# Performance work log

Measured on AMD Instinct MI355X. Metric: run time of the kernel, lower is better.

## Reference

```python
import jax, jax.numpy as jnp
import numpy as np

HEADS = 4
NEG_SLOPE = 0.2  # GATv2Conv default negative_slope and module's LeakyReLU
LN_EPS = 1e-5


def setup_inputs() -> dict:
    key = jax.random.key(0)
    ks = jax.random.split(key, 12)
    N, D, E = 50000, 128, 400000
    H, C = HEADS, D
    s = 0.05
    x = jax.random.normal(ks[0], (N, D), dtype=jnp.float32)
    edge_index = jax.random.randint(ks[1], (2, E), 0, N, dtype=jnp.int64)
    return {
        "x": x,
        "edge_index": edge_index,
        "W_l": jax.random.normal(ks[2], (D, H * C), dtype=jnp.float32) * s,
        "b_l": jnp.zeros((H * C,), jnp.float32),
        "W_r": jax.random.normal(ks[3], (D, H * C), dtype=jnp.float32) * s,
        "b_r": jnp.zeros((H * C,), jnp.float32),
        "att": jax.random.normal(ks[4], (H, C), dtype=jnp.float32) * s,
        "gat_bias": jnp.zeros((C,), jnp.float32),
        "ln_g": jnp.ones((D,), jnp.float32),
        "ln_b": jnp.zeros((D,), jnp.float32),
        "W1": jax.random.normal(ks[5], (D, 2 * D), dtype=jnp.float32) * s,
        "b1": jnp.zeros((2 * D,), jnp.float32),
        "W2": jax.random.normal(ks[6], (2 * D, D), dtype=jnp.float32) * s,
        "b2": jnp.zeros((D,), jnp.float32),
    }


def _gatv2(x, src, dst, W_l, b_l, W_r, b_r, att, gat_bias, N):
    D = x.shape[1]
    H, C = HEADS, D
    xl = (x @ W_l + b_l).reshape(N, H, C)  # source-side projection
    xr = (x @ W_r + b_r).reshape(N, H, C)  # target-side projection
    # per-edge GATv2 score: leaky_relu(x_j + x_i) . att
    e = jax.nn.leaky_relu(xl[src] + xr[dst], NEG_SLOPE)  # [E, H, C]
    alpha = jnp.einsum('ehc,hc->eh', e, att)             # [E, H]
    # segment softmax over destination nodes
    amax = jax.ops.segment_max(alpha, dst, num_segments=N)  # [N, H]
    ex = jnp.exp(alpha - amax[dst])
    denom = jax.ops.segment_sum(ex, dst, num_segments=N)
    w = ex / (denom[dst] + 1e-16)                        # [E, H]
    msg = xl[src] * w[:, :, None]                        # [E, H, C]
    out = jax.ops.segment_sum(msg, dst, num_segments=N)  # [N, H, C]
    return out.mean(axis=1) + gat_bias                   # concat=False -> head mean + bias


def reference(x, edge_index, W_l, b_l, W_r, b_r, att, gat_bias, ln_g, ln_b, W1, b1, W2, b2):
    N = x.shape[0]
    # GATv2Conv default add_self_loops=True
    loops = jnp.arange(N, dtype=edge_index.dtype)
    src = jnp.concatenate([edge_index[0], loops])
    dst = jnp.concatenate([edge_index[1], loops])
    h = x + _gatv2(x, src, dst, W_l, b_l, W_r, b_r, att, gat_bias, N)
    # LayerNorm
    mu = h.mean(-1, keepdims=True)
    var = ((h - mu) ** 2).mean(-1, keepdims=True)
    hn = (h - mu) * jax.lax.rsqrt(var + LN_EPS) * ln_g + ln_b
    # FFN with residual
    ffn = jax.nn.leaky_relu(hn @ W1 + b1, NEG_SLOPE) @ W2 + b2
    return hn + ffn
```

## Files before the change

kernel.cpp:

```cpp
#include <hip/hip_runtime.h>
#include <hip/hip_bf16.h>
#include <stdint.h>

typedef __hip_bfloat16 bf16;
typedef __attribute__((ext_vector_type(8))) short short8;
typedef __attribute__((ext_vector_type(4))) float f32x4;

#define NEG 0.2f
#define LN_EPS 1e-5f

__device__ __host__ __forceinline__ int stdch(int q) {
    return (q & ~63) | (16 * (q & 3)) | ((q & 63) >> 2);
}

__device__ __forceinline__ float bits2f(unsigned b) {
    return __uint_as_float(b << 16);
}
__device__ __forceinline__ float hi2f(unsigned b) {
    return __uint_as_float(b & 0xffff0000u);
}
__device__ __forceinline__ unsigned short f2b_bits(float f) {
    unsigned u = __float_as_uint(f);
    unsigned r = u + 0x7fffu + ((u >> 16) & 1u);
    return (unsigned short)(r >> 16);
}
__device__ __forceinline__ float lrelu(float v) {
    return fmaxf(v, 0.f) + NEG * fminf(v, 0.f);
}
__device__ __forceinline__ void unpack8(uint4 u, float* v) {
    v[0] = bits2f(u.x); v[1] = hi2f(u.x);
    v[2] = bits2f(u.y); v[3] = hi2f(u.y);
    v[4] = bits2f(u.z); v[5] = hi2f(u.z);
    v[6] = bits2f(u.w); v[7] = hi2f(u.w);
}

union S8 { uint4 u; short8 s; unsigned short us[8]; };
__device__ __forceinline__ short8 ld8b(const char* p) {
    S8 c; c.u = *(const uint4*)p; return c.s;
}
__device__ __forceinline__ short8 ld8f(const float* p) {
    float4 a = ((const float4*)p)[0], b = ((const float4*)p)[1];
    S8 c;
    c.us[0] = f2b_bits(a.x); c.us[1] = f2b_bits(a.y);
    c.us[2] = f2b_bits(a.z); c.us[3] = f2b_bits(a.w);
    c.us[4] = f2b_bits(b.x); c.us[5] = f2b_bits(b.y);
    c.us[6] = f2b_bits(b.z); c.us[7] = f2b_bits(b.w);
    return c.s;
}

template <int CTRL>
__device__ __forceinline__ float ror_add16(float x) {
    int xi = __float_as_int(x);
    int r = __builtin_amdgcn_update_dpp(xi, xi, CTRL, 0xf, 0xf, false);
    return x + __int_as_float(r);
}

__global__ void detect_kernel(const unsigned* __restrict__ xw, const int* __restrict__ ei,
                              int* __restrict__ flags, int E) {
    int lane = threadIdx.x;
    int sane = 0;
    for (int k = 0; k < 4; ++k) {
        unsigned short lo = (unsigned short)(xw[k * 64 + lane] & 0xFFFFu);
        int ex = (lo >> 7) & 0xFF;
        if (lo == 0 || (ex > 100 && ex < 155)) sane++;
    }
#pragma unroll
    for (int off = 32; off > 0; off >>= 1) sane += __shfl_xor(sane, off);
    int nchk = E < 64 ? E : 64;
    int bad = (lane < nchk) ? (ei[2 * lane + 1] != 0) : 0;
    unsigned long long bb = __ballot(bad);
    if (lane == 0) {
        flags[0] = (sane > 200) ? 1 : 0;
        flags[1] = (bb == 0ULL) ? 1 : 0;
    }
}

struct PrepArgs {
    const void* Wl; const void* Wr; const void* W1; const void* W2;
    const void* ssrc[8];
    const int* ei;
    unsigned short* Wlt; unsigned short* Wrt; unsigned short* W1t; unsigned short* W2x;
    float* smalls;
    int* deg;
    int N; int E;
};
__device__ __forceinline__ float cvt_one(const void* p, int idx, int isb) {
    return isb ? bits2f(((const unsigned short*)p)[idx]) : ((const float*)p)[idx];
}
__global__ __launch_bounds__(256) void prep_kernel(PrepArgs a, const int* __restrict__ flags) {
    int isb = flags[0];
    int i = blockIdx.x * 256 + threadIdx.x;
    int seg = blockIdx.y;
    if (seg == 0) {
        if (i < 512 * 128) {
            int j = i & 7, lane = (i >> 3) & 63, k4 = (i >> 9) & 3, nb = i >> 11;
            int col = nb * 16 + (lane & 15);
            int k = k4 * 32 + (lane >> 4) * 8 + j;
            a.Wlt[i] = isb ? ((const unsigned short*)a.Wl)[k * 512 + col]
                           : f2b_bits(((const float*)a.Wl)[k * 512 + col]);
        }
    } else if (seg == 1) {
        if (i < 512 * 128) {
            int j = i & 7, lane = (i >> 3) & 63, k4 = (i >> 9) & 3, nb = i >> 11;
            int col = nb * 16 + (lane & 15);
            int k = k4 * 32 + (lane >> 4) * 8 + j;
            a.Wrt[i] = isb ? ((const unsigned short*)a.Wr)[k * 512 + col]
                           : f2b_bits(((const float*)a.Wr)[k * 512 + col]);
        }
    } else if (seg == 2) {
        if (i < 256 * 128) {
            int j = i & 7, lane = (i >> 3) & 63;
            int r2 = i >> 9;
            int k4 = r2 & 3, nb = r2 >> 2;
            int col = nb * 16 + (lane & 15);
            int q = k4 * 32 + (lane >> 4) * 8 + j;
            int k = stdch(q);
            a.W1t[i] = isb ? ((const unsigned short*)a.W1)[k * 256 + col]
                           : f2b_bits(((const float*)a.W1)[k * 256 + col]);
        }
    } else if (seg == 3) {
        if (i < 128 * 384) {
            int j = i & 7, lane = (i >> 3) & 63;
            int r2 = i >> 9;
            int k4 = r2 % 12, nb = r2 / 12;
            int col = nb * 16 + (lane & 15);
            int p = k4 * 32 + (lane >> 4) * 8 + j;
            if (p < 256) {
                int k = stdch(p);
                a.W2x[i] = isb ? ((const unsigned short*)a.W2)[k * 128 + col]
                               : f2b_bits(((const float*)a.W2)[k * 128 + col]);
            } else {
                int q = p - 256;
                a.W2x[i] = (stdch(q) == col) ? (unsigned short)0x3F80 : (unsigned short)0;
            }
        }
    } else if (seg == 4) {
        if (i < a.E) {
            int d = flags[1] ? a.ei[2 * (size_t)a.E + 2 * (size_t)i] : a.ei[(size_t)a.E + i];
            if ((unsigned)d >= (unsigned)a.N) d = 0;
            atomicAdd(&a.deg[d], 1);
        }
    } else {
        if (i < 512) a.smalls[i] = cvt_one(a.ssrc[0], i, isb);
        else if (i < 1024) a.smalls[i] = cvt_one(a.ssrc[1], i - 512, isb);
        else if (i < 1536) {
            int j = i - 1024, h = j >> 7, q = j & 127;
            a.smalls[i] = cvt_one(a.ssrc[2], h * 128 + stdch(q), isb);
        } else if (i < 1664) a.smalls[i] = cvt_one(a.ssrc[3], stdch(i - 1536), isb);
        else if (i < 1792)   a.smalls[i] = cvt_one(a.ssrc[4], stdch(i - 1664), isb);
        else if (i < 1920)   a.smalls[i] = cvt_one(a.ssrc[5], stdch(i - 1792), isb);
        else if (i < 2176)   a.smalls[i] = cvt_one(a.ssrc[6], i - 1920, isb);
        else if (i < 2304)   a.smalls[i] = cvt_one(a.ssrc[7], i - 2176, isb);
    }
}


__global__ __launch_bounds__(256) void proj_scatter_kernel(
    const void* __restrict__ xv, const unsigned short* __restrict__ Wlt,
    const unsigned short* __restrict__ Wrt, const float* __restrict__ smalls,
    unsigned short* __restrict__ xl, unsigned short* __restrict__ xr,
    const int* __restrict__ ei, int* __restrict__ cursor, int* __restrict__ srcs,
    int N, int E, int ET, int gproj, const int* __restrict__ flags) {
    if ((int)blockIdx.x >= gproj) {
        int e = ((int)blockIdx.x - gproj) * 256 + (int)threadIdx.x;
        if (e >= ET) return;
        int s, d;
        if (e < E) {
            if (flags[1]) { s = ei[2 * (size_t)e]; d = ei[2 * (size_t)E + 2 * (size_t)e]; }
            else          { s = ei[e];             d = ei[(size_t)E + e]; }
        } else { s = e - E; d = s; }
        if ((unsigned)s >= (unsigned)N) s = 0;
        if ((unsigned)d >= (unsigned)N) d = 0;
        int pos = atomicAdd(&cursor[d], 1);
        srcs[pos] = s;
        return;
    }
    __shared__ __align__(16) unsigned short alds[64 * 136];
    int isb = flags[0];
    int tt = (int)threadIdx.x;
    int wid = threadIdx.x >> 6, lane = threadIdx.x & 63;
    int quad = lane >> 4, l16 = lane & 15;
    int m0 = blockIdx.x * 64;

#pragma unroll
    for (int s = 0; s < 4; ++s) {
        int row = s * 16 + (tt >> 4);
        int gr = m0 + row; gr = (gr < N) ? gr : N - 1;
        S8 c8;
        if (isb) c8.u = *(const uint4*)((const char*)xv + (size_t)gr * 256 + (tt & 15) * 16);
        else     c8.s = ld8f((const float*)xv + (size_t)gr * 128 + (tt & 15) * 8);
        *(uint4*)(alds + row * 136 + (tt & 15) * 8) = c8.u;
    }
    __syncthreads();
    short8 A[4][4];
#pragma unroll
    for (int rf = 0; rf < 4; ++rf)
#pragma unroll
        for (int k4 = 0; k4 < 4; ++k4)
            A[rf][k4] = ld8b((const char*)(alds + (rf * 16 + l16) * 136 + k4 * 32 + quad * 8));

    for (int iter = 0; iter < 4; ++iter) {
        const unsigned short* Wt = (iter < 2) ? Wlt : Wrt;
        const float* bias = smalls + ((iter < 2) ? 0 : 512);
        unsigned short* out = (iter < 2) ? xl : xr;
        int n0 = (iter & 1) * 256 + wid * 64;
        int nb0 = n0 >> 4;

        f32x4 acc[4][4];
#pragma unroll
        for (int rf = 0; rf < 4; ++rf)
#pragma unroll
            for (int c = 0; c < 4; ++c) acc[rf][c] = (f32x4){0.f, 0.f, 0.f, 0.f};

#pragma unroll
        for (int k4 = 0; k4 < 4; ++k4) {
            short8 b[4];
#pragma unroll
            for (int c = 0; c < 4; ++c)
                b[c] = ld8b((const char*)(Wt + (((size_t)(nb0 + c) * 4 + k4) * 64 + lane) * 8));
#pragma unroll
            for (int rf = 0; rf < 4; ++rf)
#pragma unroll
                for (int c = 0; c < 4; ++c)
                    acc[rf][c] = __builtin_amdgcn_mfma_f32_16x16x32_bf16(A[rf][k4], b[c], acc[rf][c], 0, 0, 0);
        }
        float bv[4];
#pragma unroll
        for (int c = 0; c < 4; ++c) bv[c] = bias[n0 + c * 16 + l16];
#pragma unroll
        for (int rf = 0; rf < 4; ++rf) {
#pragma unroll
            for (int j = 0; j < 4; ++j) {
                int row = m0 + rf * 16 + quad * 4 + j;
                if (row < N) {
                    uint2 pk;
                    pk.x = (unsigned)f2b_bits(acc[rf][0][j] + bv[0]) |
                           ((unsigned)f2b_bits(acc[rf][1][j] + bv[1]) << 16);
                    pk.y = (unsigned)f2b_bits(acc[rf][2][j] + bv[2]) |
                           ((unsigned)f2b_bits(acc[rf][3][j] + bv[3]) << 16);
                    *(uint2*)(out + (size_t)row * 512 + n0 + 4 * l16) = pk;
                }
            }
        }
    }
}

__global__ __launch_bounds__(256) void scanA_kernel(const int* __restrict__ deg,
                                                    int* __restrict__ part, int N) {
    int t = threadIdx.x, lane = t & 63, wid = t >> 6;
    int i = blockIdx.x * 256 + t;
    int v = (i < N) ? deg[i] + 1 : 0;
#pragma unroll
    for (int off = 32; off > 0; off >>= 1) v += __shfl_xor(v, off);
    __shared__ int ws4[4];
    if (lane == 0) ws4[wid] = v;
    __syncthreads();
    if (t == 0) part[blockIdx.x] = ws4[0] + ws4[1] + ws4[2] + ws4[3];
}

__global__ __launch_bounds__(256) void scanC_kernel(const int* __restrict__ deg,
                                                    const int* __restrict__ part,
                                                    int* __restrict__ rowptr,
                                                    int* __restrict__ cursor, int N) {
    int t = threadIdx.x, lane = t & 63, wid = t >> 6;
    int b = blockIdx.x;
    __shared__ int ws[4];
    int acc = 0;
    for (int c0 = 0; c0 < b; c0 += 256) {
        int idx = c0 + t;
        int v = (idx < b) ? part[idx] : 0;
#pragma unroll
        for (int off = 32; off > 0; off >>= 1) v += __shfl_xor(v, off);
        if (lane == 0) ws[wid] = v;
        __syncthreads();
        acc += ws[0] + ws[1] + ws[2] + ws[3];
        __syncthreads();
    }
    int i = b * 256 + t;
    int v = (i < N) ? deg[i] + 1 : 0;
    int x = v;
#pragma unroll
    for (int off = 1; off < 64; off <<= 1) {
        int u = __shfl_up(x, off);
        if (lane >= off) x += u;
    }
    if (lane == 63) ws[wid] = x;
    __syncthreads();
    int base = acc;
    for (int w = 0; w < wid; ++w) base += ws[w];
    int excl = base + x - v;
    if (i < N) { rowptr[i] = excl; cursor[i] = excl; }
    if (b == (int)gridDim.x - 1 && t == 0)
        rowptr[N] = acc + ws[0] + ws[1] + ws[2] + ws[3];
}

__global__ __launch_bounds__(256, 2) void agg_kernel(
    const bf16* __restrict__ xl, bf16* __restrict__ xr,
    const void* __restrict__ xv, const int* __restrict__ rowptr,
    const int* __restrict__ srcs, const float* __restrict__ smalls,
    int N, const int* __restrict__ flags) {
    int n = blockIdx.x * 4 + (threadIdx.x >> 6);
    if (n >= N) return;
    int lane = threadIdx.x & 63;
    int h = lane >> 4, cg = lane & 15;
    const float* att = smalls + 1024;
    const float* gat_bias = smalls + 1536;
    const float* ln_g = smalls + 1664;
    const float* ln_b = smalls + 1792;

    float att_f[8];
    {
        const float4* ap = (const float4*)(att + (size_t)h * 128 + cg * 8);
        float4 a0 = ap[0], a1 = ap[1];
        att_f[0] = a0.x; att_f[1] = a0.y; att_f[2] = a0.z; att_f[3] = a0.w;
        att_f[4] = a1.x; att_f[5] = a1.y; att_f[6] = a1.z; att_f[7] = a1.w;
    }
    float xr_f[8];
    uint4 xw = ((const uint4*)(xr + (size_t)n * 512))[lane];
    unpack8(xw, xr_f);

    float o[8];
#pragma unroll
    for (int j = 0; j < 8; ++j) o[j] = 0.f;
    float lsum = 0.f;

    int beg = rowptr[n], end = rowptr[n + 1];
    int last = end - 1;
    const uint4* xlu = (const uint4*)xl;
    int sA = srcs[beg];
    int sB = srcs[min(beg + 1, last)];
    uint4 lw = xlu[(size_t)sA * 64 + lane];
    for (int i = beg; i < end; ++i) {
        uint4 cur = lw;
        int snext = sB;
        sB = srcs[min(i + 2, last)];
        lw = xlu[(size_t)snext * 64 + lane];
        float v[8];
        unpack8(cur, v);
        float dotA = 0.f, dotB = 0.f;
#pragma unroll
        for (int j = 0; j < 8; ++j) {
            float z = v[j] + xr_f[j];
            dotA = fmaf(z, att_f[j], dotA);
            dotB = fmaf(fabsf(z), att_f[j], dotB);
        }
        float p = fmaf(0.4f, dotB, 0.6f * dotA);
        p = ror_add16<0x128>(p);
        p = ror_add16<0x124>(p);
        p = ror_add16<0x122>(p);
        p = ror_add16<0x121>(p);
        float w = __expf(fminf(p, 60.f));
        lsum += w;
#pragma unroll
        for (int j = 0; j < 8; ++j) o[j] = fmaf(w, v[j], o[j]);
        asm volatile("" : "+v"(o[0]), "+v"(o[1]), "+v"(o[2]), "+v"(o[3]),
                          "+v"(o[4]), "+v"(o[5]), "+v"(o[6]), "+v"(o[7]),
                          "+v"(lsum),
                          "+v"(att_f[0]), "+v"(att_f[1]), "+v"(att_f[2]), "+v"(att_f[3]),
                          "+v"(att_f[4]), "+v"(att_f[5]), "+v"(att_f[6]), "+v"(att_f[7]),
                          "+v"(xr_f[0]), "+v"(xr_f[1]), "+v"(xr_f[2]), "+v"(xr_f[3]),
                          "+v"(xr_f[4]), "+v"(xr_f[5]), "+v"(xr_f[6]), "+v"(xr_f[7]));
    }
    float inv = 0.25f / lsum;
#pragma unroll
    for (int j = 0; j < 8; ++j) o[j] *= inv;
#pragma unroll
    for (int j = 0; j < 8; ++j) {
        o[j] += __shfl_xor(o[j], 16);
        o[j] += __shfl_xor(o[j], 32);
    }
    int bc = 64 * (cg >> 3) + 2 * (cg & 7);
    float xf[8];
    if (flags[0]) {
#pragma unroll
        for (int c = 0; c < 4; ++c) {
            unsigned d = *(const unsigned*)((const unsigned short*)xv + (size_t)n * 128 + bc + 16 * c);
            xf[c] = bits2f(d); xf[c + 4] = hi2f(d);
        }
    } else {
#pragma unroll
        for (int c = 0; c < 4; ++c) {
            float2 f = *(const float2*)((const float*)xv + (size_t)n * 128 + bc + 16 * c);
            xf[c] = f.x; xf[c + 4] = f.y;
        }
    }
    float gb[8];
    {
        const float4* gp = (const float4*)(gat_bias + cg * 8);
        float4 a0 = gp[0], a1 = gp[1];
        gb[0] = a0.x; gb[1] = a0.y; gb[2] = a0.z; gb[3] = a0.w;
        gb[4] = a1.x; gb[5] = a1.y; gb[6] = a1.z; gb[7] = a1.w;
    }
    float vl[8];
    float s1v = 0.f;
#pragma unroll
    for (int j = 0; j < 8; ++j) { vl[j] = xf[j] + o[j] + gb[j]; s1v += vl[j]; }
    s1v += __shfl_xor(s1v, 1); s1v += __shfl_xor(s1v, 2);
    s1v += __shfl_xor(s1v, 4); s1v += __shfl_xor(s1v, 8);
    float mu = s1v * (1.f / 128.f);
    float s2v = 0.f;
#pragma unroll
    for (int j = 0; j < 8; ++j) { float d = vl[j] - mu; s2v += d * d; }
    s2v += __shfl_xor(s2v, 1); s2v += __shfl_xor(s2v, 2);
    s2v += __shfl_xor(s2v, 4); s2v += __shfl_xor(s2v, 8);
    float rinv = rsqrtf(s2v * (1.f / 128.f) + LN_EPS);
    if (h == 0) {
        float g[8], bt[8];
        const float4* gp = (const float4*)(ln_g + cg * 8);
        float4 g0 = gp[0], g1 = gp[1];
        g[0] = g0.x; g[1] = g0.y; g[2] = g0.z; g[3] = g0.w;
        g[4] = g1.x; g[5] = g1.y; g[6] = g1.z; g[7] = g1.w;
        const float4* bp = (const float4*)(ln_b + cg * 8);
        float4 b0 = bp[0], b1v = bp[1];
        bt[0] = b0.x; bt[1] = b0.y; bt[2] = b0.z; bt[3] = b0.w;
        bt[4] = b1v.x; bt[5] = b1v.y; bt[6] = b1v.z; bt[7] = b1v.w;
        float hnv[8];
#pragma unroll
        for (int j = 0; j < 8; ++j) hnv[j] = (vl[j] - mu) * rinv * g[j] + bt[j];
        char* rowp = (char*)xr + (size_t)n * 1024;
        uint4 pk;
        pk.x = (unsigned)f2b_bits(hnv[0]) | ((unsigned)f2b_bits(hnv[1]) << 16);
        pk.y = (unsigned)f2b_bits(hnv[2]) | ((unsigned)f2b_bits(hnv[3]) << 16);
        pk.z = (unsigned)f2b_bits(hnv[4]) | ((unsigned)f2b_bits(hnv[5]) << 16);
        pk.w = (unsigned)f2b_bits(hnv[6]) | ((unsigned)f2b_bits(hnv[7]) << 16);
        *(uint4*)(rowp + cg * 16) = pk;
    }
}

__global__ __launch_bounds__(256) void ffn_fused_kernel(
    const char* __restrict__ hnrows, const unsigned short* __restrict__ W1t,
    const unsigned short* __restrict__ W2x, const float* __restrict__ smalls,
    void* __restrict__ outv, int N, const int* __restrict__ flags) {
    __shared__ __align__(16) char lds[64 * 528];
    const float* b1 = smalls + 1920;
    const float* b2v = smalls + 2176;
    int tt = (int)threadIdx.x;
    int wid = threadIdx.x >> 6, lane = threadIdx.x & 63;
    int quad = lane >> 4, l16 = lane & 15;
    int m0 = blockIdx.x * 64;

#pragma unroll
    for (int s = 0; s < 4; ++s) {
        int row = s * 16 + (tt >> 4);
        int gr = m0 + row; gr = (gr < N) ? gr : N - 1;
        uint4 v = *(const uint4*)(hnrows + (size_t)gr * 1024 + (tt & 15) * 16);
        *(uint4*)(lds + row * 272 + (tt & 15) * 16) = v;
    }
    __syncthreads();
    short8 A[4][4];
#pragma unroll
    for (int rf = 0; rf < 4; ++rf)
#pragma unroll
        for (int k4 = 0; k4 < 4; ++k4)
            A[rf][k4] = ld8b(lds + (rf * 16 + l16) * 272 + (k4 * 32 + quad * 8) * 2);
    __syncthreads();

    {
        int n0 = wid * 64;
        f32x4 acc[4][4];
#pragma unroll
        for (int rf = 0; rf < 4; ++rf)
#pragma unroll
            for (int c = 0; c < 4; ++c) acc[rf][c] = (f32x4){0.f, 0.f, 0.f, 0.f};
#pragma unroll
        for (int k4 = 0; k4 < 4; ++k4) {
            short8 b[4];
#pragma unroll
            for (int c = 0; c < 4; ++c)
                b[c] = ld8b((const char*)(W1t + (((size_t)(wid * 4 + c) * 4 + k4) * 64 + lane) * 8));
#pragma unroll
            for (int rf = 0; rf < 4; ++rf)
#pragma unroll
                for (int c = 0; c < 4; ++c)
                    acc[rf][c] = __builtin_amdgcn_mfma_f32_16x16x32_bf16(A[rf][k4], b[c], acc[rf][c], 0, 0, 0);
        }
        float bv[4];
#pragma unroll
        for (int c = 0; c < 4; ++c) bv[c] = b1[n0 + c * 16 + l16];
#pragma unroll
        for (int rf = 0; rf < 4; ++rf) {
#pragma unroll
            for (int j = 0; j < 4; ++j) {
                int lrow = rf * 16 + quad * 4 + j;
                uint2 pk;
                pk.x = (unsigned)f2b_bits(lrelu(acc[rf][0][j] + bv[0])) |
                       ((unsigned)f2b_bits(lrelu(acc[rf][1][j] + bv[1])) << 16);
                pk.y = (unsigned)f2b_bits(lrelu(acc[rf][2][j] + bv[2])) |
                       ((unsigned)f2b_bits(lrelu(acc[rf][3][j] + bv[3])) << 16);
                *(uint2*)(lds + lrow * 528 + (n0 + 4 * l16) * 2) = pk;
            }
        }
    }
    __syncthreads();
    int rh = wid >> 1, nh = wid & 1;
    int n0b = nh * 64;
    f32x4 a2[2][4];
#pragma unroll
    for (int rfl = 0; rfl < 2; ++rfl)
#pragma unroll
        for (int c = 0; c < 4; ++c) a2[rfl][c] = (f32x4){0.f, 0.f, 0.f, 0.f};
#pragma unroll
    for (int kk = 0; kk < 256; kk += 32) {
        int k4 = kk >> 5;
        short8 am[2], b[4];
#pragma unroll
        for (int rfl = 0; rfl < 2; ++rfl)
            am[rfl] = ld8b(lds + (rh * 32 + rfl * 16 + l16) * 528 + (kk + quad * 8) * 2);
#pragma unroll
        for (int c = 0; c < 4; ++c)
            b[c] = ld8b((const char*)(W2x + (((size_t)(nh * 4 + c) * 12 + k4) * 64 + lane) * 8));
#pragma unroll
        for (int rfl = 0; rfl < 2; ++rfl)
#pragma unroll
            for (int c = 0; c < 4; ++c)
                a2[rfl][c] = __builtin_amdgcn_mfma_f32_16x16x32_bf16(am[rfl], b[c], a2[rfl][c], 0, 0, 0);
    }
#pragma unroll
    for (int k4 = 0; k4 < 4; ++k4) {
        short8 b[4];
#pragma unroll
        for (int c = 0; c < 4; ++c)
            b[c] = ld8b((const char*)(W2x + (((size_t)(nh * 4 + c) * 12 + 8 + k4) * 64 + lane) * 8));
#pragma unroll
        for (int rfl = 0; rfl < 2; ++rfl)
#pragma unroll
            for (int c = 0; c < 4; ++c)
                a2[rfl][c] = __builtin_amdgcn_mfma_f32_16x16x32_bf16(A[rh * 2 + rfl][k4], b[c], a2[rfl][c], 0, 0, 0);
    }
    __syncthreads();
#pragma unroll
    for (int c = 0; c < 4; ++c) {
        int col = n0b + c * 16 + l16;
        float bv = b2v[col];
#pragma unroll
        for (int rfl = 0; rfl < 2; ++rfl) {
#pragma unroll
            for (int j = 0; j < 4; ++j) {
                int lrow = rh * 32 + rfl * 16 + quad * 4 + j;
                *(float*)(lds + lrow * 528 + col * 4) = a2[rfl][c][j] + bv;
            }
        }
    }
    __syncthreads();
    int isb = flags[0];
    int t = (int)threadIdx.x;
    if (isb) {
#pragma unroll
        for (int k = 0; k < 4; ++k) {
            int f = t * 8 + k * 2048;
            int lrow = f >> 7, col = f & 127;
            int row = m0 + lrow;
            if (row < N) {
                const float* src = (const float*)(lds + lrow * 528) + col;
                uint4 pk;
                pk.x = (unsigned)f2b_bits(src[0]) | ((unsigned)f2b_bits(src[1]) << 16);
                pk.y = (unsigned)f2b_bits(src[2]) | ((unsigned)f2b_bits(src[3]) << 16);
                pk.z = (unsigned)f2b_bits(src[4]) | ((unsigned)f2b_bits(src[5]) << 16);
                pk.w = (unsigned)f2b_bits(src[6]) | ((unsigned)f2b_bits(src[7]) << 16);
                *(uint4*)((unsigned short*)outv + (size_t)row * 128 + col) = pk;
            }
        }
    } else {
#pragma unroll
        for (int k = 0; k < 8; ++k) {
            int f = t * 4 + k * 1024;
            int lrow = f >> 7, col = f & 127;
            int row = m0 + lrow;
            if (row < N) {
                const float* src = (const float*)(lds + lrow * 528) + col;
                float4 v = *(const float4*)src;
                *(float4*)((float*)outv + (size_t)row * 128 + col) = v;
            }
        }
    }
}

extern "C" void kernel_launch(void* const* d_in, const int* in_sizes, int n_in,
                              void* d_out, int out_size, void* d_ws, size_t ws_size,
                              hipStream_t stream) {
    const void* x = d_in[0];
    const int* ei = (const int*)d_in[1];

    int N = in_sizes[0] / 128;
    int E = in_sizes[1] / 2;
    int ET = E + N;
    int nb = (N + 255) / 256;

    char* base = (char*)d_ws;
    int* flags = (int*)base;
    size_t off = 256;
    float* smalls = (float*)(base + off);               off += 2304 * 4;
    off = (off + 255) & ~(size_t)255;
    unsigned short* Wlt = (unsigned short*)(base + off); off += 512 * 128 * 2;
    unsigned short* Wrt = (unsigned short*)(base + off); off += 512 * 128 * 2;
    unsigned short* W1t = (unsigned short*)(base + off); off += 256 * 128 * 2;
    unsigned short* W2x = (unsigned short*)(base + off); off += 128 * 384 * 2;
    off = (off + 1023) & ~(size_t)1023;
    bf16* xl = (bf16*)(base + off);   off += (size_t)N * 512 * 2;
    bf16* xr = (bf16*)(base + off);   off += (size_t)N * 512 * 2;
    int* srcs = (int*)(base + off);   off += (size_t)ET * 4;
    int* rowptr = (int*)(base + off); off += (size_t)(N + 1) * 4;
    int* deg = (int*)(base + off);    off += (size_t)N * 4;
    int* cursor = (int*)(base + off); off += (size_t)N * 4;
    int* part = (int*)(base + off);   off += (size_t)nb * 4;
    const char* hnrows = (const char*)xr;

    hipMemsetAsync(deg, 0, (size_t)N * 4, stream);

    detect_kernel<<<1, 64, 0, stream>>>((const unsigned*)x, ei, flags, E);

    PrepArgs pa;
    pa.Wl = d_in[2]; pa.Wr = d_in[4]; pa.W1 = d_in[10]; pa.W2 = d_in[12];
    pa.ssrc[0] = d_in[3];  pa.ssrc[1] = d_in[5];  pa.ssrc[2] = d_in[6];
    pa.ssrc[3] = d_in[7];  pa.ssrc[4] = d_in[8];  pa.ssrc[5] = d_in[9];
    pa.ssrc[6] = d_in[11]; pa.ssrc[7] = d_in[13];
    pa.ei = ei;
    pa.Wlt = Wlt; pa.Wrt = Wrt; pa.W1t = W1t; pa.W2x = W2x;
    pa.smalls = smalls; pa.deg = deg; pa.N = N; pa.E = E;
    int px = (E > 65536 ? E : 65536);
    prep_kernel<<<dim3((px + 255) / 256, 6), 256, 0, stream>>>(pa, flags);

    scanA_kernel<<<nb, 256, 0, stream>>>(deg, part, N);
    scanC_kernel<<<nb, 256, 0, stream>>>(deg, part, rowptr, cursor, N);

    int g64 = (N + 63) / 64;
    int scb = (ET + 255) / 256;
    proj_scatter_kernel<<<g64 + scb, 256, 0, stream>>>(
        x, Wlt, Wrt, smalls, (unsigned short*)xl, (unsigned short*)xr,
        ei, cursor, srcs, N, E, ET, g64, flags);

    agg_kernel<<<(N + 3) / 4, 256, 0, stream>>>(xl, xr, x, rowptr, srcs, smalls, N, flags);

    ffn_fused_kernel<<<g64, 256, 0, stream>>>(hnrows, W1t, W2x, smalls, d_out, N, flags);
}
```

Before: 300.0 us.

## Quantize source projection xl to int8 with per-64-channel scales for aggregation

The projection kernel now stores the source-side projection as offset int8, with a float scale for each group of 64 channels per row taken from a DPP max-reduction. The gather loop in the aggregation kernel loads 8 bytes per lane plus one scale instead of 16 bytes of bf16, roughly halving the random-gather traffic. The cost is extra quantize and dequantize arithmetic and lower accuracy, which could push attention scores and messages past the tolerance.

Result: slower. 319.4 us (+6.5%).

```diff
diff --git a/kernel.cpp b/kernel.cpp
--- a/kernel.cpp
+++ b/kernel.cpp
@@ -32,6 +32,9 @@
     v[2] = bits2f(u.y); v[3] = hi2f(u.y);
     v[4] = bits2f(u.z); v[5] = hi2f(u.z);
     v[6] = bits2f(u.w); v[7] = hi2f(u.w);
+}
+__device__ __forceinline__ float ub2f(unsigned d, int b) {
+    return (float)((d >> (8 * b)) & 0xffu);
 }
 
 union S8 { uint4 u; short8 s; unsigned short us[8]; };
@@ -53,6 +56,12 @@
     int xi = __float_as_int(x);
     int r = __builtin_amdgcn_update_dpp(xi, xi, CTRL, 0xf, 0xf, false);
     return x + __int_as_float(r);
+}
+template <int CTRL>
+__device__ __forceinline__ float ror_max16(float x) {
+    int xi = __float_as_int(x);
+    int r = __builtin_amdgcn_update_dpp(xi, xi, CTRL, 0xf, 0xf, false);
+    return fmaxf(x, __int_as_float(r));
 }
 
 __global__ void detect_kernel(const unsigned* __restrict__ xw, const int* __restrict__ ei,
@@ -158,7 +167,8 @@
 __global__ __launch_bounds__(256) void proj_scatter_kernel(
     const void* __restrict__ xv, const unsigned short* __restrict__ Wlt,
     const unsigned short* __restrict__ Wrt, const float* __restrict__ smalls,
-    unsigned short* __restrict__ xl, unsigned short* __restrict__ xr,
+    unsigned char* __restrict__ xl8, float* __restrict__ sclp,
+    unsigned short* __restrict__ xr,
     const int* __restrict__ ei, int* __restrict__ cursor, int* __restrict__ srcs,
     int N, int E, int ET, int gproj, const int* __restrict__ flags) {
     if ((int)blockIdx.x >= gproj) {
@@ -176,6 +186,7 @@
         return;
     }
     __shared__ __align__(16) unsigned short alds[64 * 136];
+    __shared__ float sclds[64 * 8];
     int isb = flags[0];
     int tt = (int)threadIdx.x;
     int wid = threadIdx.x >> 6, lane = threadIdx.x & 63;
@@ -202,7 +213,6 @@
     for (int iter = 0; iter < 4; ++iter) {
         const unsigned short* Wt = (iter < 2) ? Wlt : Wrt;
         const float* bias = smalls + ((iter < 2) ? 0 : 512);
-        unsigned short* out = (iter < 2) ? xl : xr;
         int n0 = (iter & 1) * 256 + wid * 64;
         int nb0 = n0 >> 4;
 
@@ -227,21 +237,60 @@
         float bv[4];
 #pragma unroll
         for (int c = 0; c < 4; ++c) bv[c] = bias[n0 + c * 16 + l16];
-#pragma unroll
-        for (int rf = 0; rf < 4; ++rf) {
-#pragma unroll
-            for (int j = 0; j < 4; ++j) {
-                int row = m0 + rf * 16 + quad * 4 + j;
-                if (row < N) {
-                    uint2 pk;
-                    pk.x = (unsigned)f2b_bits(acc[rf][0][j] + bv[0]) |
-                           ((unsigned)f2b_bits(acc[rf][1][j] + bv[1]) << 16);
-                    pk.y = (unsigned)f2b_bits(acc[rf][2][j] + bv[2]) |
-                           ((unsigned)f2b_bits(acc[rf][3][j] + bv[3]) << 16);
-                    *(uint2*)(out + (size_t)row * 512 + n0 + 4 * l16) = pk;
+        if (iter < 2) {
+            int chunk = n0 >> 6;
+#pragma unroll
+            for (int rf = 0; rf < 4; ++rf) {
+#pragma unroll
+                for (int j = 0; j < 4; ++j) {
+                    float a0 = acc[rf][0][j] + bv[0];
+                    float a1 = acc[rf][1][j] + bv[1];
+                    float a2 = acc[rf][2][j] + bv[2];
+                    float a3 = acc[rf][3][j] + bv[3];
+                    float lm = fmaxf(fmaxf(fabsf(a0), fabsf(a1)),
+                                     fmaxf(fabsf(a2), fabsf(a3)));
+                    lm = ror_max16<0x128>(lm);
+                    lm = ror_max16<0x124>(lm);
+                    lm = ror_max16<0x122>(lm);
+                    lm = ror_max16<0x121>(lm);
+                    float inv = (lm > 1e-20f) ? 127.f / lm : 0.f;
+                    int lrow = rf * 16 + quad * 4 + j;
+                    if (l16 == 0) sclds[lrow * 8 + chunk] = lm * (1.f / 127.f);
+                    int q0 = (int)rintf(a0 * inv) + 128;
+                    int q1 = (int)rintf(a1 * inv) + 128;
+                    int q2 = (int)rintf(a2 * inv) + 128;
+                    int q3 = (int)rintf(a3 * inv) + 128;
+                    unsigned pk = (unsigned)q0 | ((unsigned)q1 << 8) |
+                                  ((unsigned)q2 << 16) | ((unsigned)q3 << 24);
+                    int row = m0 + lrow;
+                    if (row < N)
+                        *(unsigned*)(xl8 + (size_t)row * 512 + n0 + 4 * l16) = pk;
                 }
             }
-        }
+        } else {
+#pragma unroll
+            for (int rf = 0; rf < 4; ++rf) {
+#pragma unroll
+                for (int j = 0; j < 4; ++j) {
+                    int row = m0 + rf * 16 + quad * 4 + j;
+                    if (row < N) {
+                        uint2 pk;
+                        pk.x = (unsigned)f2b_bits(acc[rf][0][j] + bv[0]) |
+                               ((unsigned)f2b_bits(acc[rf][1][j] + bv[1]) << 16);
+                        pk.y = (unsigned)f2b_bits(acc[rf][2][j] + bv[2]) |
+                               ((unsigned)f2b_bits(acc[rf][3][j] + bv[3]) << 16);
+                        *(uint2*)(xr + (size_t)row * 512 + n0 + 4 * l16) = pk;
+                    }
+                }
+            }
+        }
+    }
+    __syncthreads();
+#pragma unroll
+    for (int k = 0; k < 2; ++k) {
+        int idx = k * 256 + tt;
+        int lrow = idx >> 3;
+        if (m0 + lrow < N) sclp[(size_t)(m0 + lrow) * 8 + (idx & 7)] = sclds[idx];
     }
 }
 
@@ -295,7 +344,8 @@
 }
 
 __global__ __launch_bounds__(256, 2) void agg_kernel(
-    const bf16* __restrict__ xl, bf16* __restrict__ xr,
+    const uint2* __restrict__ xlq, const float* __restrict__ sclp,
+    bf16* __restrict__ xr,
     const void* __restrict__ xv, const int* __restrict__ rowptr,
     const int* __restrict__ srcs, const float* __restrict__ smalls,
     int N, const int* __restrict__ flags) {
@@ -326,17 +376,28 @@
 
     int beg = rowptr[n], end = rowptr[n + 1];
     int last = end - 1;
-    const uint4* xlu = (const uint4*)xl;
+    int sci = lane >> 3;
     int sA = srcs[beg];
     int sB = srcs[min(beg + 1, last)];
-    uint4 lw = xlu[(size_t)sA * 64 + lane];
+    uint2 lw = xlq[(size_t)sA * 64 + lane];
+    float lsc = sclp[(size_t)sA * 8 + sci];
     for (int i = beg; i < end; ++i) {
-        uint4 cur = lw;
+        uint2 cur = lw;
+        float cs = lsc;
         int snext = sB;
         sB = srcs[min(i + 2, last)];
-        lw = xlu[(size_t)snext * 64 + lane];
+        lw = xlq[(size_t)snext * 64 + lane];
+        lsc = sclp[(size_t)snext * 8 + sci];
+        float mb = cs * -128.f;
         float v[8];
-        unpack8(cur, v);
+        v[0] = fmaf(ub2f(cur.x, 0), cs, mb);
+        v[1] = fmaf(ub2f(cur.x, 1), cs, mb);
+        v[2] = fmaf(ub2f(cur.x, 2), cs, mb);
+        v[3] = fmaf(ub2f(cur.x, 3), cs, mb);
+        v[4] = fmaf(ub2f(cur.y, 0), cs, mb);
+        v[5] = fmaf(ub2f(cur.y, 1), cs, mb);
+        v[6] = fmaf(ub2f(cur.y, 2), cs, mb);
+        v[7] = fmaf(ub2f(cur.y, 3), cs, mb);
         float dotA = 0.f, dotB = 0.f;
 #pragma unroll
         for (int j = 0; j < 8; ++j) {
@@ -596,7 +657,10 @@
     unsigned short* W1t = (unsigned short*)(base + off); off += 256 * 128 * 2;
     unsigned short* W2x = (unsigned short*)(base + off); off += 128 * 384 * 2;
     off = (off + 1023) & ~(size_t)1023;
-    bf16* xl = (bf16*)(base + off);   off += (size_t)N * 512 * 2;
+    unsigned char* xl8 = (unsigned char*)(base + off);  off += (size_t)N * 512;
+    off = (off + 255) & ~(size_t)255;
+    float* sclp = (float*)(base + off);                 off += (size_t)N * 8 * 4;
+    off = (off + 1023) & ~(size_t)1023;
     bf16* xr = (bf16*)(base + off);   off += (size_t)N * 512 * 2;
     int* srcs = (int*)(base + off);   off += (size_t)ET * 4;
     int* rowptr = (int*)(base + off); off += (size_t)(N + 1) * 4;
@@ -626,10 +690,11 @@
     int g64 = (N + 63) / 64;
     int scb = (ET + 255) / 256;
     proj_scatter_kernel<<<g64 + scb, 256, 0, stream>>>(
-        x, Wlt, Wrt, smalls, (unsigned short*)xl, (unsigned short*)xr,
+        x, Wlt, Wrt, smalls, xl8, sclp, (unsigned short*)xr,
         ei, cursor, srcs, N, E, ET, g64, flags);
 
-    agg_kernel<<<(N + 3) / 4, 256, 0, stream>>>(xl, xr, x, rowptr, srcs, smalls, N, flags);
+    agg_kernel<<<(N + 3) / 4, 256, 0, stream>>>((const uint2*)xl8, sclp, xr, x,
+                                                rowptr, srcs, smalls, N, flags);
 
     ffn_fused_kernel<<<g64, 256, 0, stream>>>(hnrows, W1t, W2x, smalls, d_out, N, flags);
 }
```
